# Performance work log

Hardware: AMD Instinct MI355X
Metric: run time of the kernel (lower is better)

The kernel has to match this reference:

```python
import jax, jax.numpy as jnp
import numpy as np

SEQLEN = (512, 1024, 2048, 1536, 768, 1280, 896, 640)
HEAD_NUM = 16
HIDDEN = 1024  # head_size = 64


def setup_inputs() -> dict:
    key = jax.random.key(0)
    k1, k2 = jax.random.split(key)
    total_a = HEAD_NUM * sum(s * s for s in SEQLEN)  # packed per-seq (H, s, s) blocks
    a = jax.random.normal(k1, (total_a,), dtype=jnp.float32) * 0.02
    b = jax.random.normal(k2, (sum(SEQLEN), HIDDEN), dtype=jnp.float32)
    return {"a": a, "b": b, "seqlen": list(SEQLEN), "head_num": HEAD_NUM}


def reference(a, b, seqlen, head_num):
    """Ragged strided bmm2: per sequence i, per head h:
    C_i[:, h*hs:(h+1)*hs] = A_i[h] @ B_i[:, h*hs:(h+1)*hs].
    a packed flat as sum_i (head_num, s_i, s_i); b is (sum(s), hidden).
    """
    hidden = b.shape[1]
    hs = hidden // head_num
    outs = []
    a_off = 0
    t_off = 0
    for s in seqlen:  # static loop over ragged batch (lengths are compile-time)
        ai = jax.lax.dynamic_slice(a, (a_off,), (head_num * s * s,)).reshape(head_num, s, s)
        bi = jax.lax.dynamic_slice(b, (t_off, 0), (s, hidden)).reshape(s, head_num, hs)
        # (H, q, k) x (k, H, d) -> (q, H, d) -> (q, hidden)
        ci = jnp.einsum('hqk,khd->qhd', ai, bi).reshape(s, hidden)
        outs.append(ci)
        a_off += head_num * s * s
        t_off += s
    return jnp.concatenate(outs, axis=0)  # (sum(seqlen), hidden)
```

## Files before the change

### kernel.cpp

```cpp
#include <hip/hip_runtime.h>
#include <hip/hip_bf16.h>

typedef __attribute__((ext_vector_type(4))) float f32x4;
typedef __attribute__((ext_vector_type(8))) short bf16x8;
typedef __attribute__((ext_vector_type(4))) short bf16x4;

__device__ __forceinline__ unsigned cvt2(float lo, float hi) {
    float2 t; t.x = lo; t.y = hi;
    __hip_bfloat162 h = __float22bfloat162_rn(t);
    union { __hip_bfloat162 h; unsigned u; } c; c.h = h; return c.u;
}

__global__ __launch_bounds__(256, 4) void bmm2_k(const float* __restrict__ a,
                                                 const float* __restrict__ b,
                                                 float* __restrict__ out) {
    const int  cumblk[9] = {0,512,896,1216,1472,1696,1888,2048,2176};
    const int  slen[8]   = {2048,1536,1280,1024,896,768,640,512};
    const long aoff[8]   = {20971520,88080384,135266304,4194304,161480704,125829120,174325760,0};
    const int  toff[8]   = {1536,3584,5888,512,7168,5120,8064,0};

    __shared__ unsigned short As[2][64 * 72];
    __shared__ unsigned short Bs[2][64 * 72];

    int bid = blockIdx.x;
    int i = 0;
    #pragma unroll
    for (int t = 0; t < 7; ++t) if (bid >= cumblk[t + 1]) i = t + 1;
    int rem  = bid - cumblk[i];
    int s    = slen[i];
    int nmb  = s >> 6;
    int head = rem / nmb;
    int mb   = rem - head * nmb;

    const float* A  = a + aoff[i] + (long)head * s * s + (long)mb * 64 * s;
    const float* Bp = b + (long)toff[i] * 1024 + head * 64;
    float*       Cp = out + (long)(toff[i] + mb * 64) * 1024 + head * 64;

    int tid = threadIdx.x, lane = tid & 63, wave = tid >> 6;
    int lrow = lane & 15, lgrp = lane >> 4;

    int arow = tid >> 4;
    int kq   = tid & 15;
    const float* Ast = A + (long)arow * s + kq * 4;

    int bcol = (tid & 15) * 4;
    int btok = (tid >> 4) * 4;
    const float* Bst = Bp + (long)btok * 1024 + bcol;

    f32x4 lA0[4], lB0[4], lA1[4], lB1[4];
    f32x4 acc[4] = {};

    #pragma unroll
    for (int q = 0; q < 4; ++q) {
        lA0[q] = __builtin_nontemporal_load((const f32x4*)(Ast + (long)(16 * q) * s));
        lA1[q] = __builtin_nontemporal_load((const f32x4*)(Ast + (long)(16 * q) * s + 64));
        lB0[q] = *(const f32x4*)(Bst + (long)q * 1024);
        lB1[q] = *(const f32x4*)(Bst + (long)(64 + q) * 1024);
    }

    int NTt = s >> 6;
    for (int t = 0; t < NTt; t += 2) {
        __builtin_amdgcn_s_barrier();
        #pragma unroll
        for (int q = 0; q < 4; ++q) {
            union { bf16x4 v; unsigned u[2]; } w;
            w.u[0] = cvt2(lA0[q][0], lA0[q][1]);
            w.u[1] = cvt2(lA0[q][2], lA0[q][3]);
            *(bf16x4*)&As[0][(arow + 16 * q) * 72 + kq * 4] = w.v;
        }
        #pragma unroll
        for (int e = 0; e < 4; ++e) {
            union { bf16x4 v; unsigned u[2]; } w;
            w.u[0] = cvt2(lB0[0][e], lB0[1][e]);
            w.u[1] = cvt2(lB0[2][e], lB0[3][e]);
            *(bf16x4*)&Bs[0][(bcol + e) * 72 + btok] = w.v;
        }
        {
            long kn = (t + 2 < NTt) ? ((long)(t + 2) << 6) : 0;
            #pragma unroll
            for (int q = 0; q < 4; ++q) {
                lA0[q] = __builtin_nontemporal_load((const f32x4*)(Ast + (long)(16 * q) * s + kn));
                lB0[q] = *(const f32x4*)(Bst + (kn + q) * 1024);
            }
        }
        asm volatile("s_waitcnt lgkmcnt(0)" ::: "memory");
        __builtin_amdgcn_sched_barrier(0);
        __builtin_amdgcn_s_barrier();
        #pragma unroll
        for (int ks = 0; ks < 2; ++ks) {
            bf16x8 af = *(const bf16x8*)&As[0][(wave * 16 + lrow) * 72 + ks * 32 + lgrp * 8];
            #pragma unroll
            for (int n = 0; n < 4; ++n) {
                bf16x8 bf = *(const bf16x8*)&Bs[0][(n * 16 + lrow) * 72 + ks * 32 + lgrp * 8];
                acc[n] = __builtin_amdgcn_mfma_f32_16x16x32_bf16(af, bf, acc[n], 0, 0, 0);
            }
        }
        __builtin_amdgcn_s_barrier();
        #pragma unroll
        for (int q = 0; q < 4; ++q) {
            union { bf16x4 v; unsigned u[2]; } w;
            w.u[0] = cvt2(lA1[q][0], lA1[q][1]);
            w.u[1] = cvt2(lA1[q][2], lA1[q][3]);
            *(bf16x4*)&As[1][(arow + 16 * q) * 72 + kq * 4] = w.v;
        }
        #pragma unroll
        for (int e = 0; e < 4; ++e) {
            union { bf16x4 v; unsigned u[2]; } w;
            w.u[0] = cvt2(lB1[0][e], lB1[1][e]);
            w.u[1] = cvt2(lB1[2][e], lB1[3][e]);
            *(bf16x4*)&Bs[1][(bcol + e) * 72 + btok] = w.v;
        }
        {
            long kn = (t + 3 < NTt) ? ((long)(t + 3) << 6) : 0;
            #pragma unroll
            for (int q = 0; q < 4; ++q) {
                lA1[q] = __builtin_nontemporal_load((const f32x4*)(Ast + (long)(16 * q) * s + kn));
                lB1[q] = *(const f32x4*)(Bst + (kn + q) * 1024);
            }
        }
        asm volatile("s_waitcnt lgkmcnt(0)" ::: "memory");
        __builtin_amdgcn_sched_barrier(0);
        __builtin_amdgcn_s_barrier();
        #pragma unroll
        for (int ks = 0; ks < 2; ++ks) {
            bf16x8 af = *(const bf16x8*)&As[1][(wave * 16 + lrow) * 72 + ks * 32 + lgrp * 8];
            #pragma unroll
            for (int n = 0; n < 4; ++n) {
                bf16x8 bf = *(const bf16x8*)&Bs[1][(n * 16 + lrow) * 72 + ks * 32 + lgrp * 8];
                acc[n] = __builtin_amdgcn_mfma_f32_16x16x32_bf16(af, bf, acc[n], 0, 0, 0);
            }
        }
    }

    #pragma unroll
    for (int n = 0; n < 4; ++n)
        #pragma unroll
        for (int r = 0; r < 4; ++r) {
            int q = wave * 16 + lgrp * 4 + r;
            __builtin_nontemporal_store(acc[n][r], &Cp[(long)q * 1024 + n * 16 + lrow]);
        }
}

extern "C" void kernel_launch(void* const* d_in, const int* in_sizes, int n_in,
                              void* d_out, int out_size, void* d_ws, size_t ws_size,
                              hipStream_t stream) {
    const float* a = (const float*)d_in[0];
    const float* b = (const float*)d_in[1];
    float* out = (float*)d_out;
    bmm2_k<<<2176, 256, 0, stream>>>(a, b, out);
}
```

Baseline: 173.3 us.

## Load A fragments directly into registers, shrink B LDS tile, interleave block order

A is no longer staged through shared memory. Each lane now loads its own MFMA A fragment (8 consecutive floats) straight from global memory and converts it in registers. B is staged in a single 32-token LDS tile with a narrower padded stride, stepping K by 32 per stage instead of 64. Block IDs are remapped so that consecutive blocks are spread across eight strided chunks, presumably to balance the ragged sequences across XCDs. This drops the A LDS write/read traffic, but it doubles the number of barriers per K and makes the A global loads narrower per row, which risks worse coalescing.

```diff
diff --git a/kernel.cpp b/kernel.cpp
--- a/kernel.cpp
+++ b/kernel.cpp
@@ -3,12 +3,19 @@
 
 typedef __attribute__((ext_vector_type(4))) float f32x4;
 typedef __attribute__((ext_vector_type(8))) short bf16x8;
-typedef __attribute__((ext_vector_type(4))) short bf16x4;
+
+#define LDBK 40
 
 __device__ __forceinline__ unsigned cvt2(float lo, float hi) {
     float2 t; t.x = lo; t.y = hi;
     __hip_bfloat162 h = __float22bfloat162_rn(t);
     union { __hip_bfloat162 h; unsigned u; } c; c.h = h; return c.u;
+}
+__device__ __forceinline__ bf16x8 cvt8(f32x4 lo, f32x4 hi) {
+    union { bf16x8 v; unsigned u[4]; } r;
+    r.u[0] = cvt2(lo[0], lo[1]); r.u[1] = cvt2(lo[2], lo[3]);
+    r.u[2] = cvt2(hi[0], hi[1]); r.u[3] = cvt2(hi[2], hi[3]);
+    return r.v;
 }
 
 __global__ __launch_bounds__(256, 4) void bmm2_k(const float* __restrict__ a,
@@ -19,10 +26,10 @@
     const long aoff[8]   = {20971520,88080384,135266304,4194304,161480704,125829120,174325760,0};
     const int  toff[8]   = {1536,3584,5888,512,7168,5120,8064,0};
 
-    __shared__ unsigned short As[2][64 * 72];
-    __shared__ unsigned short Bs[2][64 * 72];
+    __shared__ unsigned short Bs[64 * LDBK];
 
-    int bid = blockIdx.x;
+    int bid = (blockIdx.x & 7) * 272 + (blockIdx.x >> 3);
+
     int i = 0;
     #pragma unroll
     for (int t = 0; t < 7; ++t) if (bid >= cumblk[t + 1]) i = t + 1;
@@ -39,94 +46,67 @@
     int tid = threadIdx.x, lane = tid & 63, wave = tid >> 6;
     int lrow = lane & 15, lgrp = lane >> 4;
 
-    int arow = tid >> 4;
-    int kq   = tid & 15;
-    const float* Ast = A + (long)arow * s + kq * 4;
+    const float* ar = A + (long)(wave * 16 + lrow) * s + lgrp * 8;
 
-    int bcol = (tid & 15) * 4;
-    int btok = (tid >> 4) * 4;
-    const float* Bst = Bp + (long)btok * 1024 + bcol;
+    int bc = (tid & 15) * 4, tok0 = (tid >> 4) * 2;
+    const float* Bst = Bp + (long)tok0 * 1024 + bc;
 
-    f32x4 lA0[4], lB0[4], lA1[4], lB1[4];
+    f32x4 aC0, aC1, aN0, aN1;
+    f32x4 lB0[2], lB1[2];
     f32x4 acc[4] = {};
 
+    int NP = s >> 5;
+
+    aC0 = __builtin_nontemporal_load((const f32x4*)(ar));
+    aC1 = __builtin_nontemporal_load((const f32x4*)(ar + 4));
     #pragma unroll
-    for (int q = 0; q < 4; ++q) {
-        lA0[q] = __builtin_nontemporal_load((const f32x4*)(Ast + (long)(16 * q) * s));
-        lA1[q] = __builtin_nontemporal_load((const f32x4*)(Ast + (long)(16 * q) * s + 64));
+    for (int q = 0; q < 2; ++q) {
         lB0[q] = *(const f32x4*)(Bst + (long)q * 1024);
-        lB1[q] = *(const f32x4*)(Bst + (long)(64 + q) * 1024);
+        lB1[q] = *(const f32x4*)(Bst + (long)(32 + q) * 1024);
     }
 
-    int NTt = s >> 6;
-    for (int t = 0; t < NTt; t += 2) {
-        __builtin_amdgcn_s_barrier();
-        #pragma unroll
-        for (int q = 0; q < 4; ++q) {
-            union { bf16x4 v; unsigned u[2]; } w;
-            w.u[0] = cvt2(lA0[q][0], lA0[q][1]);
-            w.u[1] = cvt2(lA0[q][2], lA0[q][3]);
-            *(bf16x4*)&As[0][(arow + 16 * q) * 72 + kq * 4] = w.v;
-        }
-        #pragma unroll
-        for (int e = 0; e < 4; ++e) {
-            union { bf16x4 v; unsigned u[2]; } w;
-            w.u[0] = cvt2(lB0[0][e], lB0[1][e]);
-            w.u[1] = cvt2(lB0[2][e], lB0[3][e]);
-            *(bf16x4*)&Bs[0][(bcol + e) * 72 + btok] = w.v;
-        }
+    for (int p = 0; p < NP; p += 2) {
         {
-            long kn = (t + 2 < NTt) ? ((long)(t + 2) << 6) : 0;
+            __builtin_amdgcn_s_barrier();
             #pragma unroll
-            for (int q = 0; q < 4; ++q) {
-                lA0[q] = __builtin_nontemporal_load((const f32x4*)(Ast + (long)(16 * q) * s + kn));
-                lB0[q] = *(const f32x4*)(Bst + (kn + q) * 1024);
-            }
-        }
-        asm volatile("s_waitcnt lgkmcnt(0)" ::: "memory");
-        __builtin_amdgcn_sched_barrier(0);
-        __builtin_amdgcn_s_barrier();
-        #pragma unroll
-        for (int ks = 0; ks < 2; ++ks) {
-            bf16x8 af = *(const bf16x8*)&As[0][(wave * 16 + lrow) * 72 + ks * 32 + lgrp * 8];
+            for (int e = 0; e < 4; ++e)
+                *(unsigned*)&Bs[(bc + e) * LDBK + tok0] = cvt2(lB0[0][e], lB0[1][e]);
+            long kr = (p + 2 < NP) ? (((long)p + 2) << 5) : 0;
+            #pragma unroll
+            for (int q = 0; q < 2; ++q)
+                lB0[q] = *(const f32x4*)(Bst + (kr + q) * 1024);
+            long ka = ((long)p + 1) << 5;
+            aN0 = __builtin_nontemporal_load((const f32x4*)(ar + ka));
+            aN1 = __builtin_nontemporal_load((const f32x4*)(ar + ka + 4));
+            asm volatile("s_waitcnt lgkmcnt(0)" ::: "memory");
+            __builtin_amdgcn_sched_barrier(0);
+            __builtin_amdgcn_s_barrier();
+            bf16x8 af = cvt8(aC0, aC1);
             #pragma unroll
             for (int n = 0; n < 4; ++n) {
-                bf16x8 bf = *(const bf16x8*)&Bs[0][(n * 16 + lrow) * 72 + ks * 32 + lgrp * 8];
+                bf16x8 bf = *(const bf16x8*)&Bs[(n * 16 + lrow) * LDBK + lgrp * 8];
                 acc[n] = __builtin_amdgcn_mfma_f32_16x16x32_bf16(af, bf, acc[n], 0, 0, 0);
             }
         }
-        __builtin_amdgcn_s_barrier();
-        #pragma unroll
-        for (int q = 0; q < 4; ++q) {
-            union { bf16x4 v; unsigned u[2]; } w;
-            w.u[0] = cvt2(lA1[q][0], lA1[q][1]);
-            w.u[1] = cvt2(lA1[q][2], lA1[q][3]);
-            *(bf16x4*)&As[1][(arow + 16 * q) * 72 + kq * 4] = w.v;
-        }
-        #pragma unroll
-        for (int e = 0; e < 4; ++e) {
-            union { bf16x4 v; unsigned u[2]; } w;
-            w.u[0] = cvt2(lB1[0][e], lB1[1][e]);
-            w.u[1] = cvt2(lB1[2][e], lB1[3][e]);
-            *(bf16x4*)&Bs[1][(bcol + e) * 72 + btok] = w.v;
-        }
         {
-            long kn = (t + 3 < NTt) ? ((long)(t + 3) << 6) : 0;
+            __builtin_amdgcn_s_barrier();
             #pragma unroll
-            for (int q = 0; q < 4; ++q) {
-                lA1[q] = __builtin_nontemporal_load((const f32x4*)(Ast + (long)(16 * q) * s + kn));
-                lB1[q] = *(const f32x4*)(Bst + (kn + q) * 1024);
-            }
-        }
-        asm volatile("s_waitcnt lgkmcnt(0)" ::: "memory");
-        __builtin_amdgcn_sched_barrier(0);
-        __builtin_amdgcn_s_barrier();
-        #pragma unroll
-        for (int ks = 0; ks < 2; ++ks) {
-            bf16x8 af = *(const bf16x8*)&As[1][(wave * 16 + lrow) * 72 + ks * 32 + lgrp * 8];
+            for (int e = 0; e < 4; ++e)
+                *(unsigned*)&Bs[(bc + e) * LDBK + tok0] = cvt2(lB1[0][e], lB1[1][e]);
+            long kr = (p + 3 < NP) ? (((long)p + 3) << 5) : 0;
+            #pragma unroll
+            for (int q = 0; q < 2; ++q)
+                lB1[q] = *(const f32x4*)(Bst + (kr + q) * 1024);
+            long ka = (p + 2 < NP) ? (((long)p + 2) << 5) : 0;
+            aC0 = __builtin_nontemporal_load((const f32x4*)(ar + ka));
+            aC1 = __builtin_nontemporal_load((const f32x4*)(ar + ka + 4));
+            asm volatile("s_waitcnt lgkmcnt(0)" ::: "memory");
+            __builtin_amdgcn_sched_barrier(0);
+            __builtin_amdgcn_s_barrier();
+            bf16x8 af = cvt8(aN0, aN1);
             #pragma unroll
             for (int n = 0; n < 4; ++n) {
-                bf16x8 bf = *(const bf16x8*)&Bs[1][(n * 16 + lrow) * 72 + ks * 32 + lgrp * 8];
+                bf16x8 bf = *(const bf16x8*)&Bs[(n * 16 + lrow) * LDBK + lgrp * 8];
                 acc[n] = __builtin_amdgcn_mfma_f32_16x16x32_bf16(af, bf, acc[n], 0, 0, 0);
             }
         }
```

Result: slower. 275.7 us (+59.1%).
